# Kernel optimization log

Measured on AMD Instinct MI355X. Metric: run time of the kernel, lower is better.

## Reference

```python
import jax, jax.numpy as jnp
import numpy as np

B, T, N_IN, N_HID = 512, 256, 128, 1024
FORGET_BIAS = 1.0


def setup_inputs() -> dict:
    key = jax.random.key(0)
    ks = jax.random.split(key, 5)
    x = jax.random.normal(ks[0], (B, T, N_IN), dtype=jnp.float32)
    W_hidden = jax.random.normal(ks[1], (N_IN, N_HID), dtype=jnp.float32) / np.sqrt(N_IN)
    b_hidden = jax.random.normal(ks[2], (N_HID,), dtype=jnp.float32) * 0.1
    # BasicLSTMCell kernels: [input_dim + n_hidden, 4*n_hidden], biases init to zero
    kernel1 = jax.random.normal(ks[3], (2 * N_HID, 4 * N_HID), dtype=jnp.float32) / np.sqrt(2 * N_HID)
    bias1 = jnp.zeros((4 * N_HID,), dtype=jnp.float32)
    kernel2 = jax.random.normal(ks[4], (2 * N_HID, 4 * N_HID), dtype=jnp.float32) / np.sqrt(2 * N_HID)
    bias2 = jnp.zeros((4 * N_HID,), dtype=jnp.float32)
    return {"x": x, "W_hidden": W_hidden, "b_hidden": b_hidden,
            "kernel1": kernel1, "bias1": bias1, "kernel2": kernel2, "bias2": bias2}


def _lstm_step(c, h, x_t, kernel, bias):
    # TF BasicLSTMCell gate order: i, j (cell candidate), f, o
    z = jnp.concatenate([x_t, h], axis=-1) @ kernel + bias  # [B, 4H]
    i, j, f, o = jnp.split(z, 4, axis=-1)
    new_c = c * jax.nn.sigmoid(f + FORGET_BIAS) + jax.nn.sigmoid(i) * jnp.tanh(j)
    new_h = jnp.tanh(new_c) * jax.nn.sigmoid(o)
    return new_c, new_h


def reference(x, W_hidden, b_hidden, kernel1, bias1, kernel2, bias2):
    # x: [B, T, N_IN] -> time-major [T, B, N_IN]
    xt = jnp.transpose(x, (1, 0, 2))
    # input projection + relu (batched across all time steps at once)
    proj = jax.nn.relu(xt @ W_hidden + b_hidden)  # [T, B, H]

    def step(carry, x_t):
        c1, h1, c2, h2 = carry
        c1, h1 = _lstm_step(c1, h1, x_t, kernel1, bias1)
        c2, h2 = _lstm_step(c2, h2, h1, kernel2, bias2)
        return (c1, h1, c2, h2), h2

    zeros = jnp.zeros((x.shape[0], N_HID), dtype=x.dtype)
    carry0 = (zeros, zeros, zeros, zeros)
    (_, _, _, h2_final), _ = jax.lax.scan(step, carry0, proj)
    return h2_final  # [B, N_HID], last output of top LSTM
```

## Files before the change

### kernel.cpp

```cpp
#include <hip/hip_runtime.h>
#include <cstddef>
#include <cstdint>

#define T_STEPS 256
#define BATCH   512
#define NIN     128
#define NHID    1024
#define NWGS    256

typedef _Float16 half8  __attribute__((ext_vector_type(8)));
typedef float    float4v __attribute__((ext_vector_type(4)));
typedef float    float2v __attribute__((ext_vector_type(2)));

__device__ __forceinline__ float sigmoid_f(float x) { return 1.0f / (1.0f + __expf(-x)); }
__device__ __forceinline__ float tanh_f(float x) {
    float ax = fabsf(x);
    float t  = __expf(-2.0f * ax);
    float r  = (1.0f - t) / (1.0f + t);
    return copysignf(r, x);
}

#define STORE_SC(addr, val)                                                     \
    asm volatile("global_store_dwordx4 %0, %1, off sc0 sc1"                     \
                 :: "v"((const void*)(addr)), "v"(val) : "memory")

#define WLDS_OFF  0
#define WHF_OFF   131072
#define ZS_OFF    135168
#define ZW_BYTES  2304
#define HS_OFF    153600
#define BIASG_OFF 155648
#define BH_OFF    155776
#define SMEM_BYTES 155808

__device__ __forceinline__ void grid_barrier(uint32_t* bm, uint32_t target_gen,
                                             int grp) {
    __syncthreads();
    if (threadIdx.x == 0) {
        uint32_t old = __hip_atomic_fetch_add(bm + grp * 32, 1u, __ATOMIC_RELAXED,
                                              __HIP_MEMORY_SCOPE_AGENT);
        if (old == target_gen * 32u - 1u) {
            uint32_t mold = __hip_atomic_fetch_add(bm + 256, 1u, __ATOMIC_RELAXED,
                                                   __HIP_MEMORY_SCOPE_AGENT);
            if (mold == target_gen * 8u - 1u)
                __hip_atomic_store(bm + 320, target_gen, __ATOMIC_RELAXED,
                                   __HIP_MEMORY_SCOPE_AGENT);
        }
        uint32_t spins = 0;
        while (__hip_atomic_load(bm + 320, __ATOMIC_RELAXED,
                                 __HIP_MEMORY_SCOPE_AGENT) < target_gen) {
            __builtin_amdgcn_s_sleep(8);
            if (++spins > 20000000u) break;
        }
        (void)__hip_atomic_load(bm + 320, __ATOMIC_ACQUIRE,
                                __HIP_MEMORY_SCOPE_AGENT);
    }
    __syncthreads();
}

__global__ __launch_bounds__(256)
void xconv_kernel(const float* __restrict__ x, _Float16* __restrict__ xf)
{
    __shared__ float xs[16][2][128];
    const int mt = blockIdx.x, tb = blockIdx.y;
    const int t = threadIdx.x;
    for (int tl = 0; tl < 8; ++tl) {
        __syncthreads();
#pragma unroll
        for (int i = 0; i < 4; ++i) {
            const int idx = t + i * 256;
            const int m = idx >> 6, rest = idx & 63;
            const int t2 = rest >> 5, k4 = rest & 31;
            float4v v = *(const float4v*)(x +
                ((size_t)(mt * 16 + m) * T_STEPS + (tb * 16 + tl * 2 + t2)) * NIN + k4 * 4);
            *(float4v*)&xs[m][t2][k4 * 4] = v;
        }
        __syncthreads();
#pragma unroll
        for (int i = 0; i < 2; ++i) {
            const int idx = t + i * 256;
            const int t2 = idx >> 8, rest = idx & 255;
            const int kt = rest >> 6, lane = rest & 63;
            half8 hv;
#pragma unroll
            for (int j = 0; j < 8; ++j)
                hv[j] = (_Float16)xs[lane & 15][t2][kt * 32 + (lane >> 4) * 8 + j];
            const int tg = tb * 16 + tl * 2 + t2;
            *(half8*)(xf + (((size_t)tg * 32 + mt) * 4 + kt) * 512 + lane * 8) = hv;
        }
    }
}

__global__ __launch_bounds__(512, 2)
void persist_kernel(const float* __restrict__ k1, const float* __restrict__ b1,
                    const float* __restrict__ k2, const float* __restrict__ b2,
                    const float* __restrict__ W_h, const float* __restrict__ b_h,
                    const _Float16* __restrict__ xf,
                    uint8_t* wsb, float* __restrict__ out,
                    uint32_t* barrier_mem)
{
    extern __shared__ __align__(16) char smem[];
    const size_t MB = 1024 * 1024;
    _Float16* A1b[2] = {(_Float16*)(wsb + 0 * MB), (_Float16*)(wsb + 2 * MB)};
    _Float16* A2b[2] = {(_Float16*)(wsb + 4 * MB), (_Float16*)(wsb + 6 * MB)};

    const int tid = threadIdx.x;
    const int w = tid >> 6, lane = tid & 63;
    const int q = lane >> 4, n16 = lane & 15;
    const int bid = blockIdx.x;
    const int xcd = bid & 7;
    const int layer = xcd >> 2;
    const int s = (xcd & 3) * 32 + (bid >> 3);
    const int u0 = s * 8;
    const int pu0 = s * 8;

    const float* ksrc = layer ? k2 : k1;
    const float* bsrc = layer ? b2 : b1;

    {
#pragma unroll 1
        for (int i = 0; i < 16; ++i) {
            const int kt = w * 8 + (i & 7);
            const int nt = i >> 3;
            const int colg = (nt * 2 + (n16 >> 3)) * 1024 + u0 + (n16 & 7);
            half8 hv;
#pragma unroll
            for (int j = 0; j < 8; ++j)
                hv[j] = (_Float16)ksrc[(size_t)(kt * 32 + q * 8 + j) * 4096 + colg];
            *(half8*)(smem + WLDS_OFF + (nt * 64 + kt) * 1024 + lane * 16) = hv;
        }
    }
    if (tid < 32)
        ((float*)(smem + BIASG_OFF))[tid] = bsrc[(tid >> 3) * 1024 + u0 + (tid & 7)];
    {
        if (tid < 256) {
            const int kt = tid >> 6, ln = tid & 63;
            const int nn = ln & 15;
            half8 hv;
#pragma unroll
            for (int j = 0; j < 8; ++j) {
                float v = (nn < 8)
                    ? W_h[(size_t)(kt * 32 + (ln >> 4) * 8 + j) * NHID + pu0 + nn] : 0.f;
                hv[j] = (_Float16)v;
            }
            *(half8*)(smem + WHF_OFF + kt * 1024 + ln * 16) = hv;
        }
        if (tid < 8) ((float*)(smem + BH_OFF))[tid] = b_h[pu0 + tid];
    }
    __syncthreads();

    const float* bg = (const float*)(smem + BIASG_OFF);
    const float* bh = (const float*)(smem + BH_OFF);
    float* zw = (float*)(smem + ZS_OFF + w * ZW_BYTES);
    _Float16* hw = (_Float16*)(smem + HS_OFF + w * 256);

    float cst[4][2];
#pragma unroll
    for (int mt = 0; mt < 4; ++mt) { cst[mt][0] = 0.f; cst[mt][1] = 0.f; }

    auto proj_step = [&](int tstep, _Float16* A1dst) {
        float4v pacc[2];
#pragma unroll
        for (int mi = 0; mi < 2; ++mi) pacc[mi] = (float4v){0.f, 0.f, 0.f, 0.f};
        half8 Bp[4];
        half8 Ap[4][2];
#pragma unroll
        for (int kt = 0; kt < 4; ++kt) {
            Bp[kt] = *(const half8*)(smem + WHF_OFF + kt * 1024 + lane * 16);
#pragma unroll
            for (int mi = 0; mi < 2; ++mi)
                Ap[kt][mi] = *(const half8*)(xf +
                    (((size_t)tstep * 32 + (w * 4 + layer * 2 + mi)) * 4 + kt) * 512
                    + lane * 8);
        }
#pragma unroll
        for (int kt = 0; kt < 4; ++kt)
#pragma unroll
            for (int mi = 0; mi < 2; ++mi)
                pacc[mi] = __builtin_amdgcn_mfma_f32_16x16x32_f16(Ap[kt][mi], Bp[kt], pacc[mi], 0, 0, 0);
#pragma unroll 1
        for (int mi = 0; mi < 2; ++mi) {
            if (n16 < 8) {
#pragma unroll
                for (int r = 0; r < 4; ++r)
                    zw[(q * 4 + r) * 9 + n16] = pacc[mi][r];
            }
            if (lane < 16) {
                half8 hv;
#pragma unroll
                for (int u = 0; u < 8; ++u)
                    hv[u] = (_Float16)fmaxf(zw[lane * 9 + u] + bh[u], 0.f);
                const int mtg = w * 4 + layer * 2 + mi;
                _Float16* dst = A1dst + ((size_t)mtg * 64 + (s >> 2)) * 512
                                + ((s & 3) * 16 + lane) * 8;
                STORE_SC(dst, hv);
            }
        }
    };

    auto gemm_step = [&](const _Float16* Asrc, _Float16* hdst1, _Float16* hdst2,
                         float* outp) {
        float4v acc[4][2];
#pragma unroll
        for (int mt = 0; mt < 4; ++mt) {
            acc[mt][0] = (float4v){0.f, 0.f, 0.f, 0.f};
            acc[mt][1] = (float4v){0.f, 0.f, 0.f, 0.f};
        }
        const char* aw[4];
#pragma unroll
        for (int mt = 0; mt < 4; ++mt)
            aw[mt] = (const char*)Asrc + ((size_t)(w * 4 + mt) * 64) * 1024 + lane * 16;

        half8 G0[8], G1[8], G2[8];

#define ISSUE2(buf, kb)                                                         \
        do {                                                                    \
            _Pragma("unroll")                                                   \
            for (int kk = 0; kk < 2; ++kk) {                                    \
                _Pragma("unroll")                                               \
                for (int mt = 0; mt < 4; ++mt)                                  \
                    asm volatile("global_load_dwordx4 %0, %1, off"              \
                                 : "=&v"(buf[kk * 4 + mt])                      \
                                 : "v"(aw[mt] + (size_t)((kb) + kk) * 1024));   \
            }                                                                   \
        } while (0)

#define WAITG(n, buf)                                                           \
        do {                                                                    \
            asm volatile("s_waitcnt vmcnt(" #n ")"                              \
                : "+v"(buf[0]), "+v"(buf[1]), "+v"(buf[2]), "+v"(buf[3]),       \
                  "+v"(buf[4]), "+v"(buf[5]), "+v"(buf[6]), "+v"(buf[7]));      \
            __builtin_amdgcn_sched_barrier(0);                                  \
        } while (0)

#define MFMA2(buf, kb)                                                          \
        do {                                                                    \
            _Pragma("unroll")                                                   \
            for (int kk = 0; kk < 2; ++kk) {                                    \
                half8 B0 = *(const half8*)(smem + WLDS_OFF                      \
                              + (size_t)((kb) + kk) * 1024 + lane * 16);        \
                half8 B1 = *(const half8*)(smem + WLDS_OFF + 65536              \
                              + (size_t)((kb) + kk) * 1024 + lane * 16);        \
                _Pragma("unroll")                                               \
                for (int mt = 0; mt < 4; ++mt)                                  \
                    acc[mt][0] = __builtin_amdgcn_mfma_f32_16x16x32_f16(        \
                        buf[kk * 4 + mt], B0, acc[mt][0], 0, 0, 0);             \
                _Pragma("unroll")                                               \
                for (int mt = 0; mt < 4; ++mt)                                  \
                    acc[mt][1] = __builtin_amdgcn_mfma_f32_16x16x32_f16(        \
                        buf[kk * 4 + mt], B1, acc[mt][1], 0, 0, 0);             \
            }                                                                   \
        } while (0)

        ISSUE2(G0, 0);
        ISSUE2(G1, 2);
        ISSUE2(G2, 4);
#pragma unroll 1
        for (int g3 = 0; g3 < 10; ++g3) {
            const int kb = g3 * 6;
            WAITG(16, G0);  MFMA2(G0, kb);      ISSUE2(G0, kb + 6);
            WAITG(16, G1);  MFMA2(G1, kb + 2);  ISSUE2(G1, kb + 8);
            WAITG(16, G2);  MFMA2(G2, kb + 4);
            if (g3 < 9) ISSUE2(G2, kb + 10);
        }
        WAITG(8, G0);
        MFMA2(G0, 60);
        WAITG(0, G1);
        MFMA2(G1, 62);
#undef ISSUE2
#undef WAITG
#undef MFMA2

#pragma unroll 1
        for (int mt = 0; mt < 4; ++mt) {
#pragma unroll
            for (int nt = 0; nt < 2; ++nt)
#pragma unroll
                for (int r = 0; r < 4; ++r)
                    zw[(q * 4 + r) * 36 + nt * 16 + n16] = acc[mt][nt][r];
            const float* zr = zw + n16 * 36 + q * 2;
            float2v vi = *(const float2v*)(zr + 0);
            float2v vj = *(const float2v*)(zr + 8);
            float2v vf = *(const float2v*)(zr + 16);
            float2v vo = *(const float2v*)(zr + 24);
            float hvals[2];
#pragma unroll
            for (int uu = 0; uu < 2; ++uu) {
                const int u = q * 2 + uu;
                const float zi = vi[uu] + bg[u];
                const float zj = vj[uu] + bg[8 + u];
                const float zf = vf[uu] + bg[16 + u];
                const float zo = vo[uu] + bg[24 + u];
                float c = cst[mt][uu] * sigmoid_f(zf + 1.0f) + sigmoid_f(zi) * tanh_f(zj);
                cst[mt][uu] = c;
                hvals[uu] = tanh_f(c) * sigmoid_f(zo);
            }
            hw[n16 * 8 + q * 2 + 0] = (_Float16)hvals[0];
            hw[n16 * 8 + q * 2 + 1] = (_Float16)hvals[1];
            if (outp) {
                const int row = (w * 4 + mt) * 16 + n16;
                outp[(size_t)row * NHID + u0 + q * 2 + 0] = hvals[0];
                outp[(size_t)row * NHID + u0 + q * 2 + 1] = hvals[1];
            }
            if (lane < 16) {
                half8 hv = *(half8*)(hw + lane * 8);
                const size_t loff = ((s & 3) * 16 + lane) * 8;
                const int mtg = w * 4 + mt;
                _Float16* d1 = hdst1 + ((size_t)mtg * 64 + 32 + (s >> 2)) * 512 + loff;
                STORE_SC(d1, hv);
                if (hdst2) {
                    _Float16* d2 = hdst2 + ((size_t)mtg * 64 + (s >> 2)) * 512 + loff;
                    STORE_SC(d2, hv);
                }
            }
        }
    };

    proj_step(0, A1b[0]);
    grid_barrier(barrier_mem, 1u, xcd);

    for (int p = 0; p <= 256; ++p) {
        const int pi = p & 1, po = pi ^ 1;
        if (layer == 0) {
            if (p <= 255)
                gemm_step(A1b[pi], A1b[po], A2b[po], nullptr);
        } else {
            if (p >= 1)
                gemm_step(A2b[pi], A2b[po], nullptr,
                          (p == 256) ? out : nullptr);
        }
        if (p + 1 <= 255) proj_step(p + 1, A1b[po]);
        grid_barrier(barrier_mem, (uint32_t)(p + 2), xcd);
    }
}

extern "C" void kernel_launch(void* const* d_in, const int* in_sizes, int n_in,
                              void* d_out, int out_size, void* d_ws, size_t ws_size,
                              hipStream_t stream)
{
    const float* x   = (const float*)d_in[0];
    const float* W_h = (const float*)d_in[1];
    const float* b_h = (const float*)d_in[2];
    const float* k1  = (const float*)d_in[3];
    const float* b1  = (const float*)d_in[4];
    const float* k2  = (const float*)d_in[5];
    const float* b2  = (const float*)d_in[6];
    float* out = (float*)d_out;

    const size_t MB = 1024 * 1024;
    uint8_t* wsb = (uint8_t*)d_ws;
    _Float16* xf = (_Float16*)(wsb + 8 * MB);
    uint32_t* barrier_mem = (uint32_t*)(wsb + 40 * MB);

    hipFuncSetAttribute((const void*)persist_kernel,
                        hipFuncAttributeMaxDynamicSharedMemorySize, SMEM_BYTES);

    hipMemsetAsync(wsb, 0, 8 * MB, stream);
    hipMemsetAsync(barrier_mem, 0, 4096, stream);
    xconv_kernel<<<dim3(32, 16), 256, 0, stream>>>(x, xf);
    persist_kernel<<<NWGS, 512, SMEM_BYTES, stream>>>(
        k1, b1, k2, b2, W_h, b_h, xf, wsb, out, barrier_mem);
}
```

Before: 7.538 ms.

## Prefetch projection inputs before LSTM GEMM and merge activation buffers into one layout

The x-projection loads for the next timestep are now issued before the recurrent GEMM, so their latency hides behind the GEMM instead of sitting on the critical path before the barrier. The separate layer-1 and layer-2 activation buffers are merged into one interleaved buffer per parity, with slots for the projection, h1 and h2. Layer 1 therefore writes h1 once instead of twice, and layer 2 reads its concatenated input from that shared buffer. The cost is eight extra live half8 registers during the GEMM, and correctness depends on the vmcnt waits inside the GEMM also covering the prefetched loads.

```diff
diff --git a/kernel.cpp b/kernel.cpp
--- a/kernel.cpp
+++ b/kernel.cpp
@@ -32,6 +32,10 @@
 #define BIASG_OFF 155648
 #define BH_OFF    155776
 #define SMEM_BYTES 155808
+
+#define MT_STRIDE 98304
+#define H1SLOT    32768
+#define H2SLOT    65536
 
 __device__ __forceinline__ void grid_barrier(uint32_t* bm, uint32_t target_gen,
                                              int grp) {
@@ -101,8 +105,7 @@
 {
     extern __shared__ __align__(16) char smem[];
     const size_t MB = 1024 * 1024;
-    _Float16* A1b[2] = {(_Float16*)(wsb + 0 * MB), (_Float16*)(wsb + 2 * MB)};
-    _Float16* A2b[2] = {(_Float16*)(wsb + 4 * MB), (_Float16*)(wsb + 6 * MB)};
+    char* AB[2] = {(char*)(wsb + 0 * MB), (char*)(wsb + 3 * MB)};
 
     const int tid = threadIdx.x;
     const int w = tid >> 6, lane = tid & 63;
@@ -158,26 +161,31 @@
 #pragma unroll
     for (int mt = 0; mt < 4; ++mt) { cst[mt][0] = 0.f; cst[mt][1] = 0.f; }
 
-    auto proj_step = [&](int tstep, _Float16* A1dst) {
+    half8 Pr[8];
+
+    auto proj_issue = [&](int tstep) {
+#pragma unroll
+        for (int kt = 0; kt < 4; ++kt)
+#pragma unroll
+            for (int mi = 0; mi < 2; ++mi) {
+                const char* ga = (const char*)xf +
+                    (((size_t)tstep * 32 + (w * 4 + layer * 2 + mi)) * 4 + kt) * 1024
+                    + lane * 16;
+                asm volatile("global_load_dwordx4 %0, %1, off"
+                             : "=&v"(Pr[kt * 2 + mi]) : "v"(ga));
+            }
+    };
+
+    auto proj_fin = [&](char* ABpo) {
         float4v pacc[2];
-#pragma unroll
-        for (int mi = 0; mi < 2; ++mi) pacc[mi] = (float4v){0.f, 0.f, 0.f, 0.f};
-        half8 Bp[4];
-        half8 Ap[4][2];
+        pacc[0] = (float4v){0.f, 0.f, 0.f, 0.f};
+        pacc[1] = (float4v){0.f, 0.f, 0.f, 0.f};
 #pragma unroll
         for (int kt = 0; kt < 4; ++kt) {
-            Bp[kt] = *(const half8*)(smem + WHF_OFF + kt * 1024 + lane * 16);
-#pragma unroll
-            for (int mi = 0; mi < 2; ++mi)
-                Ap[kt][mi] = *(const half8*)(xf +
-                    (((size_t)tstep * 32 + (w * 4 + layer * 2 + mi)) * 4 + kt) * 512
-                    + lane * 8);
-        }
-#pragma unroll
-        for (int kt = 0; kt < 4; ++kt)
-#pragma unroll
-            for (int mi = 0; mi < 2; ++mi)
-                pacc[mi] = __builtin_amdgcn_mfma_f32_16x16x32_f16(Ap[kt][mi], Bp[kt], pacc[mi], 0, 0, 0);
+            half8 Bp = *(const half8*)(smem + WHF_OFF + kt * 1024 + lane * 16);
+            pacc[0] = __builtin_amdgcn_mfma_f32_16x16x32_f16(Pr[kt * 2 + 0], Bp, pacc[0], 0, 0, 0);
+            pacc[1] = __builtin_amdgcn_mfma_f32_16x16x32_f16(Pr[kt * 2 + 1], Bp, pacc[1], 0, 0, 0);
+        }
 #pragma unroll 1
         for (int mi = 0; mi < 2; ++mi) {
             if (n16 < 8) {
@@ -191,15 +199,14 @@
                 for (int u = 0; u < 8; ++u)
                     hv[u] = (_Float16)fmaxf(zw[lane * 9 + u] + bh[u], 0.f);
                 const int mtg = w * 4 + layer * 2 + mi;
-                _Float16* dst = A1dst + ((size_t)mtg * 64 + (s >> 2)) * 512
-                                + ((s & 3) * 16 + lane) * 8;
+                char* dst = ABpo + (size_t)mtg * MT_STRIDE
+                            + (s >> 2) * 1024 + ((s & 3) * 16 + lane) * 16;
                 STORE_SC(dst, hv);
             }
         }
     };
 
-    auto gemm_step = [&](const _Float16* Asrc, _Float16* hdst1, _Float16* hdst2,
-                         float* outp) {
+    auto gemm_step = [&](const char* Abase, char* ABpo, int hslot, float* outp) {
         float4v acc[4][2];
 #pragma unroll
         for (int mt = 0; mt < 4; ++mt) {
@@ -209,7 +216,7 @@
         const char* aw[4];
 #pragma unroll
         for (int mt = 0; mt < 4; ++mt)
-            aw[mt] = (const char*)Asrc + ((size_t)(w * 4 + mt) * 64) * 1024 + lane * 16;
+            aw[mt] = Abase + (size_t)(w * 4 + mt) * MT_STRIDE + lane * 16;
 
         half8 G0[8], G1[8], G2[8];
 
@@ -304,32 +311,44 @@
             }
             if (lane < 16) {
                 half8 hv = *(half8*)(hw + lane * 8);
-                const size_t loff = ((s & 3) * 16 + lane) * 8;
                 const int mtg = w * 4 + mt;
-                _Float16* d1 = hdst1 + ((size_t)mtg * 64 + 32 + (s >> 2)) * 512 + loff;
+                char* d1 = ABpo + (size_t)mtg * MT_STRIDE + hslot
+                           + (s >> 2) * 1024 + ((s & 3) * 16 + lane) * 16;
                 STORE_SC(d1, hv);
-                if (hdst2) {
-                    _Float16* d2 = hdst2 + ((size_t)mtg * 64 + (s >> 2)) * 512 + loff;
-                    STORE_SC(d2, hv);
-                }
             }
         }
     };
 
-    proj_step(0, A1b[0]);
+    proj_issue(0);
+    asm volatile("s_waitcnt vmcnt(0)");
+    __builtin_amdgcn_sched_barrier(0);
+    proj_fin(AB[0]);
     grid_barrier(barrier_mem, 1u, xcd);
 
     for (int p = 0; p <= 256; ++p) {
         const int pi = p & 1, po = pi ^ 1;
+        const bool dop = (p + 1 <= 255);
+        if (dop) proj_issue(p + 1);
+        bool didGemm = false;
         if (layer == 0) {
-            if (p <= 255)
-                gemm_step(A1b[pi], A1b[po], A2b[po], nullptr);
+            if (p <= 255) {
+                gemm_step(AB[pi], AB[po], H1SLOT, nullptr);
+                didGemm = true;
+            }
         } else {
-            if (p >= 1)
-                gemm_step(A2b[pi], A2b[po], nullptr,
+            if (p >= 1) {
+                gemm_step(AB[pi] + H1SLOT, AB[po], H2SLOT,
                           (p == 256) ? out : nullptr);
-        }
-        if (p + 1 <= 255) proj_step(p + 1, A1b[po]);
+                didGemm = true;
+            }
+        }
+        if (dop) {
+            if (!didGemm) {
+                asm volatile("s_waitcnt vmcnt(0)");
+                __builtin_amdgcn_sched_barrier(0);
+            }
+            proj_fin(AB[po]);
+        }
         grid_barrier(barrier_mem, (uint32_t)(p + 2), xcd);
     }
 }
@@ -355,7 +374,7 @@
     hipFuncSetAttribute((const void*)persist_kernel,
                         hipFuncAttributeMaxDynamicSharedMemorySize, SMEM_BYTES);
 
-    hipMemsetAsync(wsb, 0, 8 * MB, stream);
+    hipMemsetAsync(wsb, 0, 6 * MB, stream);
     hipMemsetAsync(barrier_mem, 0, 4096, stream);
     xconv_kernel<<<dim3(32, 16), 256, 0, stream>>>(x, xf);
     persist_kernel<<<NWGS, 512, SMEM_BYTES, stream>>>(
```

Result: faster. 7.267 ms (-3.6%).
